# Optimization experiments

Measured on AMD Instinct MI355X. Metric: run time of the kernel, lower is better.

Reference implementation:

```python
import jax, jax.numpy as jnp
import numpy as np

DIM, HIDDEN, E = 1024, 4096, 8
B, L = 2, 2048


def setup_inputs() -> dict:
    key = jax.random.key(0)
    ks = jax.random.split(key, 6)
    s_in = 1.0 / np.sqrt(DIM)
    s_h = 1.0 / np.sqrt(HIDDEN)
    return {
        "x": jax.random.normal(ks[0], (B, L, DIM), dtype=jnp.float32),
        "Wg": jax.random.uniform(ks[1], (E, DIM), jnp.float32, -s_in, s_in),
        "W1": jax.random.uniform(ks[2], (E, DIM, HIDDEN), jnp.float32, -s_in, s_in),
        "b1": jax.random.uniform(ks[3], (E, HIDDEN), jnp.float32, -s_in, s_in),
        "W2": jax.random.uniform(ks[4], (E, HIDDEN, DIM), jnp.float32, -s_h, s_h),
        "b2": jax.random.uniform(ks[5], (E, DIM), jnp.float32, -s_h, s_h),
    }


def reference(x, Wg, W1, b1, W2, b2):
    # Router: top-1 over gate logits (softmax is monotone, argmax of probs == argmax of logits)
    gate_logits = jnp.einsum("bld,ed->ble", x, Wg)  # [B, L, E]
    top1 = jnp.argmax(gate_logits, axis=-1)          # [B, L] int
    out = jnp.zeros_like(x)
    # Fixed small loop over experts (structurally distinct weights); per-expert
    # dense MLP + select, honoring top-1 dispatch/combine semantics.
    for e in range(E):
        mask = (top1 == e)[..., None]                                   # [B, L, 1]
        h = jax.nn.gelu(jnp.einsum("bld,dh->blh", x, W1[e]) + b1[e],
                        approximate=False)                              # [B, L, H]
        y = jnp.einsum("blh,hd->bld", h, W2[e]) + b2[e]                 # [B, L, D]
        out = jnp.where(mask, y, out)
    return out
```

## Files before the change

### kernel.cpp

```cpp
#include <hip/hip_runtime.h>
#include <hip/hip_bf16.h>
#include <math.h>

#define NTOK 4096
#define DIMSZ 1024
#define HID 4096
#define NE 8
#define RT_MAX 40

typedef unsigned short u16;
typedef unsigned int u32;
typedef __attribute__((ext_vector_type(8))) short bf16x8;
typedef __attribute__((ext_vector_type(4))) float f32x4;

#define SWZ(r) (((r) >> 1) & 3)

static __device__ __forceinline__ u16 f2bf(float f) {
    u32 u = __float_as_uint(f);
    u32 r = u + 0x7fffu + ((u >> 16) & 1u);
    return (u16)(r >> 16);
}

static __device__ __forceinline__ u32 pk2bf(float lo, float hi) {
    __hip_bfloat162 h = __float22bfloat162_rn(make_float2(lo, hi));
    return *(u32*)&h;
}

__global__ void k_init(int* counts, int* cursor) {
    if (threadIdx.x < NE) { counts[threadIdx.x] = 0; cursor[threadIdx.x] = 0; }
}

__global__ void k_zero(float* p) {
    int i = blockIdx.x * 1024 + threadIdx.x * 4;
    *(float4*)(p + i) = make_float4(0.f, 0.f, 0.f, 0.f);
}

__global__ __launch_bounds__(256) void k_router(const float* __restrict__ x,
                                                const float* __restrict__ Wg,
                                                int* __restrict__ ids,
                                                int* __restrict__ counts) {
    int wave = threadIdx.x >> 6;
    int lane = threadIdx.x & 63;
    int t = blockIdx.x * 4 + wave;

    const float4* xr = (const float4*)(x + (size_t)t * DIMSZ);
    float4 xv[4];
#pragma unroll
    for (int j = 0; j < 4; j++) xv[j] = xr[j * 64 + lane];

    float s[NE];
#pragma unroll
    for (int e = 0; e < NE; e++) {
        const float4* wr = (const float4*)(Wg + (size_t)e * DIMSZ);
        float p = 0.f;
#pragma unroll
        for (int j = 0; j < 4; j++) {
            float4 w = wr[j * 64 + lane];
            p += xv[j].x * w.x + xv[j].y * w.y + xv[j].z * w.z + xv[j].w * w.w;
        }
#pragma unroll
        for (int m = 32; m >= 1; m >>= 1) p += __shfl_xor(p, m, 64);
        s[e] = p;
    }
    if (lane == 0) {
        int best = 0;
#pragma unroll
        for (int e = 1; e < NE; e++) if (s[e] > s[best]) best = e;
        ids[t] = best;
        atomicAdd(&counts[best], 1);
    }
}

__global__ void k_scan(const int* __restrict__ counts, int* __restrict__ offs) {
    if (threadIdx.x == 0) {
        int a = 0;
        for (int e = 0; e < NE; e++) { offs[e] = a; a += counts[e]; }
    }
}

__global__ __launch_bounds__(256) void k_gather(const float* __restrict__ x,
                                                const int* __restrict__ ids,
                                                const int* __restrict__ offs,
                                                int* __restrict__ cursor,
                                                int* __restrict__ perm,
                                                u16* __restrict__ Xg) {
    int t = blockIdx.x;
    __shared__ int sp;
    if (threadIdx.x == 0) {
        int e = ids[t];
        int p = offs[e] + atomicAdd(&cursor[e], 1);
        perm[p] = t;
        sp = p;
    }
    __syncthreads();
    int p = sp;
    const float4* src = (const float4*)(x + (size_t)t * DIMSZ);
    float4 v = src[threadIdx.x];
    u32 w0 = pk2bf(v.x, v.y);
    u32 w1 = pk2bf(v.z, v.w);
    uint2* dst = (uint2*)(Xg + (size_t)p * DIMSZ + threadIdx.x * 4);
    *dst = make_uint2(w0, w1);
}

__global__ __launch_bounds__(256) void k_wt(const float* __restrict__ W1,
                                            const float* __restrict__ W2,
                                            u16* __restrict__ W1T,
                                            u16* __restrict__ W2T) {
    int bid = blockIdx.x;
    const float* src;
    u16* dst;
    int K, N, kt, nt;
    if (bid < 8192) {
        int e = bid >> 10, t = bid & 1023;
        kt = t >> 6; nt = t & 63;
        src = W1 + (size_t)e * 1024 * 4096;
        dst = W1T + (size_t)e * 4096 * 1024;
        K = 1024; N = 4096;
    } else {
        int b = bid - 8192;
        int e = b >> 10, t = b & 1023;
        kt = t >> 4; nt = t & 15;
        src = W2 + (size_t)e * 4096 * 1024;
        dst = W2T + (size_t)e * 1024 * 4096;
        K = 4096; N = 1024;
    }
    __shared__ u32 T[32][65];
    int tid = threadIdx.x;
#pragma unroll
    for (int pass = 0; pass < 2; pass++) {
        int kp = (tid >> 4) + pass * 16;
        int nc = (tid & 15) * 4;
        const float* r0 = src + (size_t)(kt * 64 + 2 * kp) * N + nt * 64 + nc;
        float4 a = *(const float4*)r0;
        float4 b = *(const float4*)(r0 + N);
        T[kp][nc + 0] = pk2bf(a.x, b.x);
        T[kp][nc + 1] = pk2bf(a.y, b.y);
        T[kp][nc + 2] = pk2bf(a.z, b.z);
        T[kp][nc + 3] = pk2bf(a.w, b.w);
    }
    __syncthreads();
    int n = tid >> 2;
    int sb = (tid & 3) * 8;
    u16* orow = dst + (size_t)(nt * 64 + n) * K + kt * 64;
#pragma unroll
    for (int p = 0; p < 2; p++) {
        int s = sb + p * 4;
        uint4 w = make_uint4(T[s][n], T[s + 1][n], T[s + 2][n], T[s + 3][n]);
        *(uint4*)(orow + 2 * s) = w;
    }
}

template <int KDIM, int NDIM, int EPI, int KSPLIT>
__global__ __launch_bounds__(256, 3) void k_gemm(const u16* __restrict__ A,
                                                 const u16* __restrict__ Wt,
                                                 const float* __restrict__ biasAll,
                                                 const int* __restrict__ counts,
                                                 const int* __restrict__ offs,
                                                 const int* __restrict__ perm,
                                                 u16* __restrict__ Hout,
                                                 float* __restrict__ Fout) {
    constexpr int NT = NDIM / 128;
    constexpr int NREST = NT * KSPLIT;
    constexpr int NWG = RT_MAX * NREST;
    constexpr int CPX = NWG / 8;
    constexpr int KL = KDIM / KSPLIT;
    constexpr int NKL = KL / 32;
    int bid = blockIdx.x;
    int wid = (bid & 7) * CPX + (bid >> 3);
    int x = wid / NREST;
    int rest = wid % NREST;
    int ks = rest % KSPLIT;
    int n0 = (rest / KSPLIT) * 128;
    int kbase = ks * KL;

    int e = -1, lrt = 0, a0 = 0;
#pragma unroll
    for (int i = 0; i < NE; i++) {
        int rt = (counts[i] + 127) >> 7;
        if (e < 0 && x < a0 + rt) { e = i; lrt = x - a0; }
        a0 += rt;
    }
    if (e < 0) return;
    int row0 = offs[e] + lrt * 128;
    int nrows = offs[e] + counts[e] - row0;
    if (nrows > 128) nrows = 128;

    __shared__ alignas(16) u16 Asb[3][128][32];
    __shared__ alignas(16) u16 Bsb[3][128][32];

    int tid = threadIdx.x;
    int lane = tid & 63;
    int wave = tid >> 6;
    int wr = wave >> 1, wc = wave & 1;

    const u16* srcA[2];
    const u16* srcB[2];
#pragma unroll
    for (int p = 0; p < 2; p++) {
        int g = p * 256 + tid;
        int r = g >> 2, slot = g & 3;
        int rc = r < nrows ? r : nrows - 1;
        int kg = (slot ^ SWZ(r)) * 8;
        srcA[p] = A + (size_t)(row0 + rc) * KDIM + kbase + kg;
        srcB[p] = Wt + (size_t)e * NDIM * KDIM + (size_t)(n0 + r) * KDIM + kbase + kg;
    }

    f32x4 acc[4][4] = {};
    int fr = lane & 15, fc = lane >> 4;

    u16 *A0 = &Asb[0][0][0], *A1 = &Asb[1][0][0], *A2 = &Asb[2][0][0];
    u16 *B0 = &Bsb[0][0][0], *B1 = &Bsb[1][0][0], *B2 = &Bsb[2][0][0];

#define STAGE(AD, BD, KT)                                                       \
    {                                                                           \
        _Pragma("unroll")                                                       \
        for (int p = 0; p < 2; p++) {                                           \
            __builtin_amdgcn_global_load_lds(                                   \
                (const __attribute__((address_space(1))) void*)(srcA[p] + (size_t)(KT) * 32), \
                (__attribute__((address_space(3))) void*)((AD) + (p * 256 + wave * 64) * 8), \
                16, 0, 0);                                                      \
            __builtin_amdgcn_global_load_lds(                                   \
                (const __attribute__((address_space(1))) void*)(srcB[p] + (size_t)(KT) * 32), \
                (__attribute__((address_space(3))) void*)((BD) + (p * 256 + wave * 64) * 8), \
                16, 0, 0);                                                      \
        }                                                                       \
    }

#define COMPUTE(AP, BP)                                                         \
    {                                                                           \
        bf16x8 af[4], bfr[4];                                                   \
        _Pragma("unroll")                                                       \
        for (int m = 0; m < 4; m++) {                                           \
            int r = wr * 64 + m * 16 + fr;                                      \
            af[m] = *(const bf16x8*)((AP) + r * 32 + (fc ^ SWZ(r)) * 8);        \
        }                                                                       \
        _Pragma("unroll")                                                       \
        for (int n = 0; n < 4; n++) {                                           \
            int N = wc * 64 + n * 16 + fr;                                      \
            bfr[n] = *(const bf16x8*)((BP) + N * 32 + (fc ^ SWZ(N)) * 8);       \
        }                                                                       \
        _Pragma("unroll")                                                       \
        for (int m = 0; m < 4; m++)                                             \
            _Pragma("unroll")                                                   \
            for (int n = 0; n < 4; n++)                                         \
                acc[m][n] = __builtin_amdgcn_mfma_f32_16x16x32_bf16(af[m], bfr[n], acc[m][n], 0, 0, 0); \
    }

#define WAITV(N) asm volatile("s_waitcnt vmcnt(" #N ")" ::: "memory")
#define BAR()    __builtin_amdgcn_s_barrier()
#define SBAR()   __builtin_amdgcn_sched_barrier(0)

    STAGE(A0, B0, 0);
    STAGE(A1, B1, 1);

    for (int kk = 0; kk < NKL - 2; kk++) {
        WAITV(4);
        BAR();
        SBAR();
        STAGE(A2, B2, kk + 2);
        COMPUTE(A0, B0);
        u16* t;
        t = A0; A0 = A1; A1 = A2; A2 = t;
        t = B0; B0 = B1; B1 = B2; B2 = t;
    }
    WAITV(4);
    BAR();
    SBAR();
    COMPUTE(A0, B0);
    WAITV(0);
    BAR();
    SBAR();
    COMPUTE(A1, B1);

#undef STAGE
#undef COMPUTE
#undef WAITV
#undef BAR
#undef SBAR

    int cb = lane & 15;
    int rq = lane >> 4;
#pragma unroll
    for (int m = 0; m < 4; m++) {
        int rbase = wr * 64 + m * 16 + rq * 4;
#pragma unroll
        for (int n = 0; n < 4; n++) {
            int col = n0 + wc * 64 + n * 16 + cb;
            float bias = (EPI == 2 && ks != 0) ? 0.f : biasAll[(size_t)e * NDIM + col];
#pragma unroll
            for (int j = 0; j < 4; j++) {
                int r = rbase + j;
                if (r < nrows) {
                    float v = acc[m][n][j] + bias;
                    int p = row0 + r;
                    if (EPI == 1) {
                        float g = 0.5f * v * (1.0f + erff(v * 0.70710678118654752f));
                        Hout[(size_t)p * NDIM + col] = f2bf(g);
                    } else {
                        int trow = perm[p];
                        atomicAdd(&Fout[(size_t)trow * NDIM + col], v);
                    }
                }
            }
        }
    }
}

extern "C" void kernel_launch(void* const* d_in, const int* in_sizes, int n_in,
                              void* d_out, int out_size, void* d_ws, size_t ws_size,
                              hipStream_t stream) {
    const float* x  = (const float*)d_in[0];
    const float* Wg = (const float*)d_in[1];
    const float* W1 = (const float*)d_in[2];
    const float* b1 = (const float*)d_in[3];
    const float* W2 = (const float*)d_in[4];
    const float* b2 = (const float*)d_in[5];
    float* out = (float*)d_out;

    char* ws = (char*)d_ws;
    int* ids    = (int*)(ws + 0);
    int* counts = (int*)(ws + 16384);
    int* offs   = (int*)(ws + 16448);
    int* cursor = (int*)(ws + 16512);
    int* perm   = (int*)(ws + 16576);

    u16* Xg   = (u16*)(ws + 65536);
    u16* H    = (u16*)(ws + 65536 + 8388608);
    u16* W1T  = (u16*)(ws + 65536 + 8388608 + 33554432);
    u16* W2T  = (u16*)(ws + 65536 + 8388608 + 33554432 + 67108864);

    k_init<<<dim3(1), dim3(64), 0, stream>>>(counts, cursor);
    k_router<<<dim3(NTOK / 4), dim3(256), 0, stream>>>(x, Wg, ids, counts);
    k_scan<<<dim3(1), dim3(64), 0, stream>>>(counts, offs);
    k_gather<<<dim3(NTOK), dim3(256), 0, stream>>>(x, ids, offs, cursor, perm, Xg);
    k_wt<<<dim3(16384), dim3(256), 0, stream>>>(W1, W2, W1T, W2T);
    k_zero<<<dim3(NTOK * DIMSZ / 1024), dim3(256), 0, stream>>>(out);
    k_gemm<DIMSZ, HID, 1, 1><<<dim3(RT_MAX * (HID / 128)), dim3(256), 0, stream>>>(
        Xg, W1T, b1, counts, offs, perm, H, (float*)nullptr);
    k_gemm<HID, DIMSZ, 2, 2><<<dim3(RT_MAX * (DIMSZ / 128) * 2), dim3(256), 0, stream>>>(
        H, W2T, b2, counts, offs, perm, (u16*)nullptr, out);
}
```

Baseline: 365.7 us.

## Enlarge grouped GEMM tiles to 256x256 with 8-wave blocks and split-K pipelining

Both expert GEMMs now use 256x256 output tiles computed by 512-thread blocks. Each wave owns a 128x64 sub-tile, and a K-tile of 64 is split into two 32-wide halves that are double-buffered in LDS. Loads for the next halves are interleaved between MFMA phases, and s_setprio raises priority around the MFMA bursts. The intent is to raise arithmetic intensity and cut global and LDS traffic per FLOP. In exchange, larger tiles waste more work on partially filled expert row tiles, launch fewer workgroups, and add more barriers per K step.

Result: slower. 429.3 us (+17.4%).

```diff
diff --git a/kernel.cpp b/kernel.cpp
--- a/kernel.cpp
+++ b/kernel.cpp
@@ -6,14 +6,15 @@
 #define DIMSZ 1024
 #define HID 4096
 #define NE 8
-#define RT_MAX 40
+#define RT2 24
 
 typedef unsigned short u16;
 typedef unsigned int u32;
 typedef __attribute__((ext_vector_type(8))) short bf16x8;
 typedef __attribute__((ext_vector_type(4))) float f32x4;
 
-#define SWZ(r) (((r) >> 1) & 3)
+#define AS1 __attribute__((address_space(1)))
+#define AS3 __attribute__((address_space(3)))
 
 static __device__ __forceinline__ u16 f2bf(float f) {
     u32 u = __float_as_uint(f);
@@ -96,10 +97,8 @@
     int p = sp;
     const float4* src = (const float4*)(x + (size_t)t * DIMSZ);
     float4 v = src[threadIdx.x];
-    u32 w0 = pk2bf(v.x, v.y);
-    u32 w1 = pk2bf(v.z, v.w);
     uint2* dst = (uint2*)(Xg + (size_t)p * DIMSZ + threadIdx.x * 4);
-    *dst = make_uint2(w0, w1);
+    *dst = make_uint2(pk2bf(v.x, v.y), pk2bf(v.z, v.w));
 }
 
 __global__ __launch_bounds__(256) void k_wt(const float* __restrict__ W1,
@@ -145,13 +144,12 @@
 #pragma unroll
     for (int p = 0; p < 2; p++) {
         int s = sb + p * 4;
-        uint4 w = make_uint4(T[s][n], T[s + 1][n], T[s + 2][n], T[s + 3][n]);
-        *(uint4*)(orow + 2 * s) = w;
+        *(uint4*)(orow + 2 * s) = make_uint4(T[s][n], T[s + 1][n], T[s + 2][n], T[s + 3][n]);
     }
 }
 
 template <int KDIM, int NDIM, int EPI, int KSPLIT>
-__global__ __launch_bounds__(256, 3) void k_gemm(const u16* __restrict__ A,
+__global__ __launch_bounds__(512, 2) void k_gemm(const u16* __restrict__ A,
                                                  const u16* __restrict__ Wt,
                                                  const float* __restrict__ biasAll,
                                                  const int* __restrict__ counts,
@@ -159,130 +157,148 @@
                                                  const int* __restrict__ perm,
                                                  u16* __restrict__ Hout,
                                                  float* __restrict__ Fout) {
-    constexpr int NT = NDIM / 128;
+    constexpr int NT = NDIM / 256;
     constexpr int NREST = NT * KSPLIT;
-    constexpr int NWG = RT_MAX * NREST;
+    constexpr int NWG = RT2 * NREST;
     constexpr int CPX = NWG / 8;
     constexpr int KL = KDIM / KSPLIT;
-    constexpr int NKL = KL / 32;
+    constexpr int NKT = KL / 64;
+
     int bid = blockIdx.x;
     int wid = (bid & 7) * CPX + (bid >> 3);
     int x = wid / NREST;
     int rest = wid % NREST;
     int ks = rest % KSPLIT;
-    int n0 = (rest / KSPLIT) * 128;
+    int n0 = (rest / KSPLIT) * 256;
     int kbase = ks * KL;
 
     int e = -1, lrt = 0, a0 = 0;
 #pragma unroll
     for (int i = 0; i < NE; i++) {
-        int rt = (counts[i] + 127) >> 7;
+        int rt = (counts[i] + 255) >> 8;
         if (e < 0 && x < a0 + rt) { e = i; lrt = x - a0; }
         a0 += rt;
     }
     if (e < 0) return;
-    int row0 = offs[e] + lrt * 128;
+    int row0 = offs[e] + lrt * 256;
     int nrows = offs[e] + counts[e] - row0;
-    if (nrows > 128) nrows = 128;
-
-    __shared__ alignas(16) u16 Asb[3][128][32];
-    __shared__ alignas(16) u16 Bsb[3][128][32];
+    if (nrows > 256) nrows = 256;
+
+    __shared__ u16 Ls[2][2][2][256][32];
 
     int tid = threadIdx.x;
     int lane = tid & 63;
     int wave = tid >> 6;
-    int wr = wave >> 1, wc = wave & 1;
-
-    const u16* srcA[2];
-    const u16* srcB[2];
-#pragma unroll
-    for (int p = 0; p < 2; p++) {
-        int g = p * 256 + tid;
+    int wr = wave >> 2;
+    int wc = wave & 3;
+    int fr = lane & 15, fc = lane >> 4;
+    int gsl = fc ^ ((fr >> 1) & 3);
+
+    const u16 *sA[2], *sB[2];
+#pragma unroll
+    for (int c = 0; c < 2; c++) {
+        int g = c * 512 + tid;
         int r = g >> 2, slot = g & 3;
-        int rc = r < nrows ? r : nrows - 1;
-        int kg = (slot ^ SWZ(r)) * 8;
-        srcA[p] = A + (size_t)(row0 + rc) * KDIM + kbase + kg;
-        srcB[p] = Wt + (size_t)e * NDIM * KDIM + (size_t)(n0 + r) * KDIM + kbase + kg;
-    }
-
-    f32x4 acc[4][4] = {};
-    int fr = lane & 15, fc = lane >> 4;
-
-    u16 *A0 = &Asb[0][0][0], *A1 = &Asb[1][0][0], *A2 = &Asb[2][0][0];
-    u16 *B0 = &Bsb[0][0][0], *B1 = &Bsb[1][0][0], *B2 = &Bsb[2][0][0];
-
-#define STAGE(AD, BD, KT)                                                       \
-    {                                                                           \
-        _Pragma("unroll")                                                       \
-        for (int p = 0; p < 2; p++) {                                           \
-            __builtin_amdgcn_global_load_lds(                                   \
-                (const __attribute__((address_space(1))) void*)(srcA[p] + (size_t)(KT) * 32), \
-                (__attribute__((address_space(3))) void*)((AD) + (p * 256 + wave * 64) * 8), \
-                16, 0, 0);                                                      \
-            __builtin_amdgcn_global_load_lds(                                   \
-                (const __attribute__((address_space(1))) void*)(srcB[p] + (size_t)(KT) * 32), \
-                (__attribute__((address_space(3))) void*)((BD) + (p * 256 + wave * 64) * 8), \
-                16, 0, 0);                                                      \
-        }                                                                       \
-    }
-
-#define COMPUTE(AP, BP)                                                         \
-    {                                                                           \
-        bf16x8 af[4], bfr[4];                                                   \
-        _Pragma("unroll")                                                       \
-        for (int m = 0; m < 4; m++) {                                           \
-            int r = wr * 64 + m * 16 + fr;                                      \
-            af[m] = *(const bf16x8*)((AP) + r * 32 + (fc ^ SWZ(r)) * 8);        \
-        }                                                                       \
-        _Pragma("unroll")                                                       \
-        for (int n = 0; n < 4; n++) {                                           \
-            int N = wc * 64 + n * 16 + fr;                                      \
-            bfr[n] = *(const bf16x8*)((BP) + N * 32 + (fc ^ SWZ(N)) * 8);       \
-        }                                                                       \
-        _Pragma("unroll")                                                       \
-        for (int m = 0; m < 4; m++)                                             \
-            _Pragma("unroll")                                                   \
-            for (int n = 0; n < 4; n++)                                         \
-                acc[m][n] = __builtin_amdgcn_mfma_f32_16x16x32_bf16(af[m], bfr[n], acc[m][n], 0, 0, 0); \
-    }
-
-#define WAITV(N) asm volatile("s_waitcnt vmcnt(" #N ")" ::: "memory")
-#define BAR()    __builtin_amdgcn_s_barrier()
-#define SBAR()   __builtin_amdgcn_sched_barrier(0)
-
-    STAGE(A0, B0, 0);
-    STAGE(A1, B1, 1);
-
-    for (int kk = 0; kk < NKL - 2; kk++) {
-        WAITV(4);
-        BAR();
-        SBAR();
-        STAGE(A2, B2, kk + 2);
-        COMPUTE(A0, B0);
-        u16* t;
-        t = A0; A0 = A1; A1 = A2; A2 = t;
-        t = B0; B0 = B1; B1 = B2; B2 = t;
-    }
-    WAITV(4);
-    BAR();
-    SBAR();
-    COMPUTE(A0, B0);
-    WAITV(0);
-    BAR();
-    SBAR();
-    COMPUTE(A1, B1);
-
-#undef STAGE
-#undef COMPUTE
-#undef WAITV
+        int rc = r < nrows ? r : (nrows - 1);
+        int kg = (slot ^ ((r >> 1) & 3)) * 8;
+        sA[c] = A + (size_t)(row0 + rc) * KDIM + kbase + kg;
+        sB[c] = Wt + (size_t)e * NDIM * KDIM + (size_t)(n0 + r) * KDIM + kbase + kg;
+    }
+
+    f32x4 acc[8][4] = {};
+    bf16x8 bfr[4];
+
+#define STG(OP, SRC, BUF, S, KT)                                                  \
+    if ((KT) < NKT) {                                                             \
+        __builtin_amdgcn_global_load_lds(                                         \
+            (const AS1 void*)((SRC)[0] + (size_t)(KT) * 64 + (S) * 32),           \
+            (AS3 void*)(&Ls[BUF][OP][S][0][0] + (wave * 64) * 8), 16, 0, 0);      \
+        __builtin_amdgcn_global_load_lds(                                         \
+            (const AS1 void*)((SRC)[1] + (size_t)(KT) * 64 + (S) * 32),           \
+            (AS3 void*)(&Ls[BUF][OP][S][0][0] + (512 + wave * 64) * 8), 16, 0, 0);\
+    }
+
+#define LDA(BUF, S, H, AF)                                                        \
+    _Pragma("unroll")                                                             \
+    for (int m = 0; m < 4; m++)                                                   \
+        AF[m] = *(const bf16x8*)(&Ls[BUF][0][S][0][0] +                           \
+                 (wr * 128 + (H) * 64 + m * 16 + fr) * 32 + gsl * 8);
+
+#define LDB(BUF, S)                                                               \
+    _Pragma("unroll")                                                             \
+    for (int n = 0; n < 4; n++)                                                   \
+        bfr[n] = *(const bf16x8*)(&Ls[BUF][1][S][0][0] +                          \
+                 (wc * 64 + n * 16 + fr) * 32 + gsl * 8);
+
+#define MM(H, AF)                                                                 \
+    __builtin_amdgcn_s_setprio(1);                                                \
+    _Pragma("unroll")                                                             \
+    for (int m = 0; m < 4; m++)                                                   \
+        _Pragma("unroll")                                                         \
+        for (int n = 0; n < 4; n++)                                               \
+            acc[(H) * 4 + m][n] = __builtin_amdgcn_mfma_f32_16x16x32_bf16(        \
+                AF[m], bfr[n], acc[(H) * 4 + m][n], 0, 0, 0);                     \
+    __builtin_amdgcn_s_setprio(0);
+
+#define WL()  asm volatile("s_waitcnt lgkmcnt(0)" ::: "memory")
+#define BAR() __builtin_amdgcn_s_barrier()
+#define SCB() __builtin_amdgcn_sched_barrier(0)
+
+#define KTILE(BUF, OBUF, KT, GATE)                                                \
+    {                                                                             \
+        bf16x8 af[4];                                                             \
+                                                                          \
+        GATE; BAR(); SCB();                                                       \
+        LDA(BUF, 0, 0, af); LDB(BUF, 0);                                          \
+        STG(0, sA, OBUF, 1, (KT) + 1);                                            \
+        WL(); SCB(); MM(0, af); BAR();                                            \
+                                                                          \
+        LDA(BUF, 0, 1, af);                                                       \
+        STG(1, sB, OBUF, 1, (KT) + 1);                                            \
+        BAR(); WL(); SCB(); MM(1, af); BAR();                                     \
+                                                                          \
+        LDA(BUF, 1, 0, af); LDB(BUF, 1);                                          \
+        STG(0, sA, BUF, 0, (KT) + 2);                                             \
+        BAR(); WL(); SCB(); MM(0, af); BAR();                                     \
+                                                                          \
+        LDA(BUF, 1, 1, af);                                                       \
+        STG(1, sB, BUF, 0, (KT) + 2);                                             \
+        BAR(); WL(); SCB(); MM(1, af); BAR();                                     \
+    }
+
+#define GATE4 asm volatile("s_waitcnt vmcnt(4)" ::: "memory")
+#define GATE0 asm volatile("s_waitcnt vmcnt(0)" ::: "memory")
+
+    STG(0, sA, 0, 0, 0);
+    STG(1, sB, 0, 0, 0);
+    STG(0, sA, 0, 1, 0);
+    STG(1, sB, 0, 1, 0);
+    STG(0, sA, 1, 0, 1);
+    STG(1, sB, 1, 0, 1);
+
+    for (int t = 0; t + 3 < NKT; t += 2) {
+        KTILE(0, 1, t, GATE4);
+        KTILE(1, 0, t + 1, GATE4);
+    }
+    KTILE(0, 1, NKT - 2, GATE4);
+    KTILE(1, 0, NKT - 1, GATE0);
+
+#undef STG
+#undef LDA
+#undef LDB
+#undef MM
+#undef WL
 #undef BAR
-#undef SBAR
+#undef SCB
+#undef KTILE
+#undef GATE4
+#undef GATE0
 
     int cb = lane & 15;
     int rq = lane >> 4;
 #pragma unroll
-    for (int m = 0; m < 4; m++) {
-        int rbase = wr * 64 + m * 16 + rq * 4;
+    for (int am = 0; am < 8; am++) {
+        int rbase = wr * 128 + (am >> 2) * 64 + (am & 3) * 16 + rq * 4;
 #pragma unroll
         for (int n = 0; n < 4; n++) {
             int col = n0 + wc * 64 + n * 16 + cb;
@@ -291,14 +307,13 @@
             for (int j = 0; j < 4; j++) {
                 int r = rbase + j;
                 if (r < nrows) {
-                    float v = acc[m][n][j] + bias;
+                    float v = acc[am][n][j] + bias;
                     int p = row0 + r;
                     if (EPI == 1) {
                         float g = 0.5f * v * (1.0f + erff(v * 0.70710678118654752f));
                         Hout[(size_t)p * NDIM + col] = f2bf(g);
                     } else {
-                        int trow = perm[p];
-                        atomicAdd(&Fout[(size_t)trow * NDIM + col], v);
+                        atomicAdd(&Fout[(size_t)perm[p] * NDIM + col], v);
                     }
                 }
             }
@@ -335,8 +350,8 @@
     k_gather<<<dim3(NTOK), dim3(256), 0, stream>>>(x, ids, offs, cursor, perm, Xg);
     k_wt<<<dim3(16384), dim3(256), 0, stream>>>(W1, W2, W1T, W2T);
     k_zero<<<dim3(NTOK * DIMSZ / 1024), dim3(256), 0, stream>>>(out);
-    k_gemm<DIMSZ, HID, 1, 1><<<dim3(RT_MAX * (HID / 128)), dim3(256), 0, stream>>>(
+    k_gemm<DIMSZ, HID, 1, 1><<<dim3(RT2 * (HID / 256)), dim3(512), 0, stream>>>(
         Xg, W1T, b1, counts, offs, perm, H, (float*)nullptr);
-    k_gemm<HID, DIMSZ, 2, 2><<<dim3(RT_MAX * (DIMSZ / 128) * 2), dim3(256), 0, stream>>>(
+    k_gemm<HID, DIMSZ, 2, 2><<<dim3(RT2 * (DIMSZ / 256) * 2), dim3(512), 0, stream>>>(
         H, W2T, b2, counts, offs, perm, (u16*)nullptr, out);
 }
```

## Fuse prep kernels, overlap W2 transpose with GEMM1, double-buffer GEMMs

Applied to the files above, without the earlier changes.

Cuts the launch count by merging the gather with the W1 transpose, and merging GEMM1 with the W2 transpose and output zeroing into one grid. Per-expert offsets are now computed inline from the counts, which removes the scan kernel. The GEMM pipeline drops from triple to double buffering with an extra barrier, so LDS use falls and occupancy is raised to 5. GEMM2 split-K goes from 2 to 4. Risks are a more serialised load/compute pipeline and more output atomics.

New measurement: 453.8 us. 1.24x slower.

```diff
diff --git a/kernel.cpp b/kernel.cpp
--- a/kernel.cpp
+++ b/kernel.cpp
@@ -13,6 +13,9 @@
 typedef __attribute__((ext_vector_type(8))) short bf16x8;
 typedef __attribute__((ext_vector_type(4))) float f32x4;
 
+#define AS1 __attribute__((address_space(1)))
+#define AS3 __attribute__((address_space(3)))
+
 #define SWZ(r) (((r) >> 1) & 3)
 
 static __device__ __forceinline__ u16 f2bf(float f) {
@@ -24,15 +27,6 @@
 static __device__ __forceinline__ u32 pk2bf(float lo, float hi) {
     __hip_bfloat162 h = __float22bfloat162_rn(make_float2(lo, hi));
     return *(u32*)&h;
-}
-
-__global__ void k_init(int* counts, int* cursor) {
-    if (threadIdx.x < NE) { counts[threadIdx.x] = 0; cursor[threadIdx.x] = 0; }
-}
-
-__global__ void k_zero(float* p) {
-    int i = blockIdx.x * 1024 + threadIdx.x * 4;
-    *(float4*)(p + i) = make_float4(0.f, 0.f, 0.f, 0.f);
 }
 
 __global__ __launch_bounds__(256) void k_router(const float* __restrict__ x,
@@ -71,60 +65,10 @@
     }
 }
 
-__global__ void k_scan(const int* __restrict__ counts, int* __restrict__ offs) {
-    if (threadIdx.x == 0) {
-        int a = 0;
-        for (int e = 0; e < NE; e++) { offs[e] = a; a += counts[e]; }
-    }
-}
-
-__global__ __launch_bounds__(256) void k_gather(const float* __restrict__ x,
-                                                const int* __restrict__ ids,
-                                                const int* __restrict__ offs,
-                                                int* __restrict__ cursor,
-                                                int* __restrict__ perm,
-                                                u16* __restrict__ Xg) {
-    int t = blockIdx.x;
-    __shared__ int sp;
-    if (threadIdx.x == 0) {
-        int e = ids[t];
-        int p = offs[e] + atomicAdd(&cursor[e], 1);
-        perm[p] = t;
-        sp = p;
-    }
-    __syncthreads();
-    int p = sp;
-    const float4* src = (const float4*)(x + (size_t)t * DIMSZ);
-    float4 v = src[threadIdx.x];
-    u32 w0 = pk2bf(v.x, v.y);
-    u32 w1 = pk2bf(v.z, v.w);
-    uint2* dst = (uint2*)(Xg + (size_t)p * DIMSZ + threadIdx.x * 4);
-    *dst = make_uint2(w0, w1);
-}
-
-__global__ __launch_bounds__(256) void k_wt(const float* __restrict__ W1,
-                                            const float* __restrict__ W2,
-                                            u16* __restrict__ W1T,
-                                            u16* __restrict__ W2T) {
-    int bid = blockIdx.x;
-    const float* src;
-    u16* dst;
-    int K, N, kt, nt;
-    if (bid < 8192) {
-        int e = bid >> 10, t = bid & 1023;
-        kt = t >> 6; nt = t & 63;
-        src = W1 + (size_t)e * 1024 * 4096;
-        dst = W1T + (size_t)e * 4096 * 1024;
-        K = 1024; N = 4096;
-    } else {
-        int b = bid - 8192;
-        int e = b >> 10, t = b & 1023;
-        kt = t >> 4; nt = t & 15;
-        src = W2 + (size_t)e * 4096 * 1024;
-        dst = W2T + (size_t)e * 1024 * 4096;
-        K = 4096; N = 1024;
-    }
-    __shared__ u32 T[32][65];
+static __device__ __forceinline__ void wt_body(const float* __restrict__ src,
+                                               u16* __restrict__ dst,
+                                               int K, int N, int kt, int nt,
+                                               u32 (*T)[65]) {
     int tid = threadIdx.x;
 #pragma unroll
     for (int pass = 0; pass < 2; pass++) {
@@ -145,27 +89,26 @@
 #pragma unroll
     for (int p = 0; p < 2; p++) {
         int s = sb + p * 4;
-        uint4 w = make_uint4(T[s][n], T[s + 1][n], T[s + 2][n], T[s + 3][n]);
-        *(uint4*)(orow + 2 * s) = w;
+        *(uint4*)(orow + 2 * s) = make_uint4(T[s][n], T[s + 1][n], T[s + 2][n], T[s + 3][n]);
     }
 }
 
 template <int KDIM, int NDIM, int EPI, int KSPLIT>
-__global__ __launch_bounds__(256, 3) void k_gemm(const u16* __restrict__ A,
+static __device__ __forceinline__ void gemm_body(int bid,
+                                                 const u16* __restrict__ A,
                                                  const u16* __restrict__ Wt,
                                                  const float* __restrict__ biasAll,
                                                  const int* __restrict__ counts,
-                                                 const int* __restrict__ offs,
                                                  const int* __restrict__ perm,
                                                  u16* __restrict__ Hout,
-                                                 float* __restrict__ Fout) {
+                                                 float* __restrict__ Fout,
+                                                 u16* lds ) {
     constexpr int NT = NDIM / 128;
     constexpr int NREST = NT * KSPLIT;
     constexpr int NWG = RT_MAX * NREST;
     constexpr int CPX = NWG / 8;
     constexpr int KL = KDIM / KSPLIT;
     constexpr int NKL = KL / 32;
-    int bid = blockIdx.x;
     int wid = (bid & 7) * CPX + (bid >> 3);
     int x = wid / NREST;
     int rest = wid % NREST;
@@ -173,20 +116,22 @@
     int n0 = (rest / KSPLIT) * 128;
     int kbase = ks * KL;
 
-    int e = -1, lrt = 0, a0 = 0;
+    int e = -1, lrt = 0, a0 = 0, off_e = 0, cum = 0;
 #pragma unroll
     for (int i = 0; i < NE; i++) {
-        int rt = (counts[i] + 127) >> 7;
-        if (e < 0 && x < a0 + rt) { e = i; lrt = x - a0; }
+        int c = counts[i];
+        int rt = (c + 127) >> 7;
+        if (e < 0 && x < a0 + rt) { e = i; lrt = x - a0; off_e = cum; }
         a0 += rt;
+        cum += c;
     }
     if (e < 0) return;
-    int row0 = offs[e] + lrt * 128;
-    int nrows = offs[e] + counts[e] - row0;
+    int row0 = off_e + lrt * 128;
+    int nrows = off_e + counts[e] - row0;
     if (nrows > 128) nrows = 128;
 
-    __shared__ alignas(16) u16 Asb[3][128][32];
-    __shared__ alignas(16) u16 Bsb[3][128][32];
+    u16* Asb[2] = { lds,        lds + 8192 };
+    u16* Bsb[2] = { lds + 4096, lds + 12288 };
 
     int tid = threadIdx.x;
     int lane = tid & 63;
@@ -208,36 +153,31 @@
     f32x4 acc[4][4] = {};
     int fr = lane & 15, fc = lane >> 4;
 
-    u16 *A0 = &Asb[0][0][0], *A1 = &Asb[1][0][0], *A2 = &Asb[2][0][0];
-    u16 *B0 = &Bsb[0][0][0], *B1 = &Bsb[1][0][0], *B2 = &Bsb[2][0][0];
-
-#define STAGE(AD, BD, KT)                                                       \
+#define STAGE(BUF, KT)                                                          \
     {                                                                           \
         _Pragma("unroll")                                                       \
         for (int p = 0; p < 2; p++) {                                           \
             __builtin_amdgcn_global_load_lds(                                   \
-                (const __attribute__((address_space(1))) void*)(srcA[p] + (size_t)(KT) * 32), \
-                (__attribute__((address_space(3))) void*)((AD) + (p * 256 + wave * 64) * 8), \
-                16, 0, 0);                                                      \
+                (const AS1 void*)(srcA[p] + (size_t)(KT) * 32),                 \
+                (AS3 void*)(Asb[BUF] + (p * 256 + wave * 64) * 8), 16, 0, 0);   \
             __builtin_amdgcn_global_load_lds(                                   \
-                (const __attribute__((address_space(1))) void*)(srcB[p] + (size_t)(KT) * 32), \
-                (__attribute__((address_space(3))) void*)((BD) + (p * 256 + wave * 64) * 8), \
-                16, 0, 0);                                                      \
+                (const AS1 void*)(srcB[p] + (size_t)(KT) * 32),                 \
+                (AS3 void*)(Bsb[BUF] + (p * 256 + wave * 64) * 8), 16, 0, 0);   \
         }                                                                       \
     }
 
-#define COMPUTE(AP, BP)                                                         \
+#define COMPUTE(BUF)                                                            \
     {                                                                           \
         bf16x8 af[4], bfr[4];                                                   \
         _Pragma("unroll")                                                       \
         for (int m = 0; m < 4; m++) {                                           \
             int r = wr * 64 + m * 16 + fr;                                      \
-            af[m] = *(const bf16x8*)((AP) + r * 32 + (fc ^ SWZ(r)) * 8);        \
+            af[m] = *(const bf16x8*)(Asb[BUF] + r * 32 + (fc ^ SWZ(r)) * 8);    \
         }                                                                       \
         _Pragma("unroll")                                                       \
         for (int n = 0; n < 4; n++) {                                           \
             int N = wc * 64 + n * 16 + fr;                                      \
-            bfr[n] = *(const bf16x8*)((BP) + N * 32 + (fc ^ SWZ(N)) * 8);       \
+            bfr[n] = *(const bf16x8*)(Bsb[BUF] + N * 32 + (fc ^ SWZ(N)) * 8);   \
         }                                                                       \
         _Pragma("unroll")                                                       \
         for (int m = 0; m < 4; m++)                                             \
@@ -248,35 +188,28 @@
 
 #define WAITV(N) asm volatile("s_waitcnt vmcnt(" #N ")" ::: "memory")
 #define BAR()    __builtin_amdgcn_s_barrier()
-#define SBAR()   __builtin_amdgcn_sched_barrier(0)
-
-    STAGE(A0, B0, 0);
-    STAGE(A1, B1, 1);
-
-    for (int kk = 0; kk < NKL - 2; kk++) {
+#define SCB()    __builtin_amdgcn_sched_barrier(0)
+
+    STAGE(0, 0);
+    for (int kk = 0; kk < NKL - 1; kk++) {
+        STAGE((kk + 1) & 1, kk + 1);
         WAITV(4);
         BAR();
-        SBAR();
-        STAGE(A2, B2, kk + 2);
-        COMPUTE(A0, B0);
-        u16* t;
-        t = A0; A0 = A1; A1 = A2; A2 = t;
-        t = B0; B0 = B1; B1 = B2; B2 = t;
-    }
-    WAITV(4);
-    BAR();
-    SBAR();
-    COMPUTE(A0, B0);
+        SCB();
+        COMPUTE(kk & 1);
+        BAR();
+        SCB();
+    }
     WAITV(0);
     BAR();
-    SBAR();
-    COMPUTE(A1, B1);
+    SCB();
+    COMPUTE((NKL - 1) & 1);
 
 #undef STAGE
 #undef COMPUTE
 #undef WAITV
 #undef BAR
-#undef SBAR
+#undef SCB
 
     int cb = lane & 15;
     int rq = lane >> 4;
@@ -297,13 +230,84 @@
                         float g = 0.5f * v * (1.0f + erff(v * 0.70710678118654752f));
                         Hout[(size_t)p * NDIM + col] = f2bf(g);
                     } else {
-                        int trow = perm[p];
-                        atomicAdd(&Fout[(size_t)trow * NDIM + col], v);
+                        atomicAdd(&Fout[(size_t)perm[p] * NDIM + col], v);
                     }
                 }
             }
         }
     }
+}
+
+__global__ __launch_bounds__(256) void k_pre(const float* __restrict__ x,
+                                             const int* __restrict__ ids,
+                                             const int* __restrict__ counts,
+                                             int* __restrict__ cursor,
+                                             int* __restrict__ perm,
+                                             u16* __restrict__ Xg,
+                                             const float* __restrict__ W1,
+                                             u16* __restrict__ W1T) {
+    __shared__ u32 T[32][65];
+    __shared__ int sp;
+    int bid = blockIdx.x;
+    if (bid < NTOK) {
+        int t = bid;
+        if (threadIdx.x == 0) {
+            int e = ids[t];
+            int off = 0;
+            for (int i = 0; i < e; i++) off += counts[i];
+            int p = off + atomicAdd(&cursor[e], 1);
+            perm[p] = t;
+            sp = p;
+        }
+        __syncthreads();
+        int p = sp;
+        float4 v = ((const float4*)(x + (size_t)t * DIMSZ))[threadIdx.x];
+        *(uint2*)(Xg + (size_t)p * DIMSZ + threadIdx.x * 4) =
+            make_uint2(pk2bf(v.x, v.y), pk2bf(v.z, v.w));
+    } else {
+        int b = bid - NTOK;
+        int e = b >> 10, t = b & 1023;
+        int kt = t >> 6, nt = t & 63;
+        wt_body(W1 + (size_t)e * 1024 * 4096, W1T + (size_t)e * 4096 * 1024,
+                1024, 4096, kt, nt, T);
+    }
+}
+
+__global__ __launch_bounds__(256, 5) void k_mid(const u16* __restrict__ Xg,
+                                                const u16* __restrict__ W1T,
+                                                const float* __restrict__ b1,
+                                                const int* __restrict__ counts,
+                                                const int* __restrict__ perm,
+                                                u16* __restrict__ H,
+                                                const float* __restrict__ W2,
+                                                u16* __restrict__ W2T,
+                                                float* __restrict__ out) {
+    __shared__ alignas(16) u16 LDS[16384];
+    int bid = blockIdx.x;
+    if (bid < 1280) {
+        gemm_body<DIMSZ, HID, 1, 1>(bid, Xg, W1T, b1, counts, perm, H, (float*)nullptr, LDS);
+    } else if (bid < 1280 + 8192) {
+        int b = bid - 1280;
+        int e = b >> 10, t = b & 1023;
+        int kt = t >> 4, nt = t & 15;
+        wt_body(W2 + (size_t)e * 4096 * 1024, W2T + (size_t)e * 1024 * 4096,
+                4096, 1024, kt, nt, (u32(*)[65])LDS);
+    } else {
+        int b = bid - (1280 + 8192);
+        int i = b * 1024 + threadIdx.x * 4;
+        *(float4*)(out + i) = make_float4(0.f, 0.f, 0.f, 0.f);
+    }
+}
+
+__global__ __launch_bounds__(256, 5) void k_g2(const u16* __restrict__ H,
+                                               const u16* __restrict__ W2T,
+                                               const float* __restrict__ b2,
+                                               const int* __restrict__ counts,
+                                               const int* __restrict__ perm,
+                                               float* __restrict__ out) {
+    __shared__ alignas(16) u16 LDS[16384];
+    gemm_body<HID, DIMSZ, 2, 4>(blockIdx.x, H, W2T, b2, counts, perm,
+                                (u16*)nullptr, out, LDS);
 }
 
 extern "C" void kernel_launch(void* const* d_in, const int* in_sizes, int n_in,
@@ -320,7 +324,6 @@
     char* ws = (char*)d_ws;
     int* ids    = (int*)(ws + 0);
     int* counts = (int*)(ws + 16384);
-    int* offs   = (int*)(ws + 16448);
     int* cursor = (int*)(ws + 16512);
     int* perm   = (int*)(ws + 16576);
 
@@ -329,14 +332,9 @@
     u16* W1T  = (u16*)(ws + 65536 + 8388608 + 33554432);
     u16* W2T  = (u16*)(ws + 65536 + 8388608 + 33554432 + 67108864);
 
-    k_init<<<dim3(1), dim3(64), 0, stream>>>(counts, cursor);
+    hipMemsetAsync(ws + 16384, 0, 192, stream);
     k_router<<<dim3(NTOK / 4), dim3(256), 0, stream>>>(x, Wg, ids, counts);
-    k_scan<<<dim3(1), dim3(64), 0, stream>>>(counts, offs);
-    k_gather<<<dim3(NTOK), dim3(256), 0, stream>>>(x, ids, offs, cursor, perm, Xg);
-    k_wt<<<dim3(16384), dim3(256), 0, stream>>>(W1, W2, W1T, W2T);
-    k_zero<<<dim3(NTOK * DIMSZ / 1024), dim3(256), 0, stream>>>(out);
-    k_gemm<DIMSZ, HID, 1, 1><<<dim3(RT_MAX * (HID / 128)), dim3(256), 0, stream>>>(
-        Xg, W1T, b1, counts, offs, perm, H, (float*)nullptr);
-    k_gemm<HID, DIMSZ, 2, 2><<<dim3(RT_MAX * (DIMSZ / 128) * 2), dim3(256), 0, stream>>>(
-        H, W2T, b2, counts, offs, perm, (u16*)nullptr, out);
-}
+    k_pre<<<dim3(NTOK + 8192), dim3(256), 0, stream>>>(x, ids, counts, cursor, perm, Xg, W1, W1T);
+    k_mid<<<dim3(1280 + 8192 + 4096), dim3(256), 0, stream>>>(Xg, W1T, b1, counts, perm, H, W2, W2T, out);
+    k_g2<<<dim3(1280), dim3(256), 0, stream>>>(H, W2T, b2, counts, perm, out);
+}
```

## Enlarge expert GEMM row tile to 256 with 512-thread workgroups

Applied to the files above, without the earlier changes.

Doubles the M tile of both expert GEMMs from 128 to 256 rows, using 8 waves per workgroup so each weight tile loaded into LDS is reused across twice as many token rows. The load staging is reorganized (two A loads and one B load per thread per stage) and the vmcnt wait adjusted accordingly. This reduces weight traffic per output, but adds more padded rows for experts with partial tiles, fewer workgroups, and larger LDS use per block.

Measured after the change: 370.8 us. No clear change (+1.4%).

```diff
diff --git a/kernel.cpp b/kernel.cpp
--- a/kernel.cpp
+++ b/kernel.cpp
@@ -6,12 +6,15 @@
 #define DIMSZ 1024
 #define HID 4096
 #define NE 8
-#define RT_MAX 40
+#define RT256 24
 
 typedef unsigned short u16;
 typedef unsigned int u32;
 typedef __attribute__((ext_vector_type(8))) short bf16x8;
 typedef __attribute__((ext_vector_type(4))) float f32x4;
+
+#define AS1 __attribute__((address_space(1)))
+#define AS3 __attribute__((address_space(3)))
 
 #define SWZ(r) (((r) >> 1) & 3)
 
@@ -94,12 +97,9 @@
     }
     __syncthreads();
     int p = sp;
-    const float4* src = (const float4*)(x + (size_t)t * DIMSZ);
-    float4 v = src[threadIdx.x];
-    u32 w0 = pk2bf(v.x, v.y);
-    u32 w1 = pk2bf(v.z, v.w);
-    uint2* dst = (uint2*)(Xg + (size_t)p * DIMSZ + threadIdx.x * 4);
-    *dst = make_uint2(w0, w1);
+    float4 v = ((const float4*)(x + (size_t)t * DIMSZ))[threadIdx.x];
+    *(uint2*)(Xg + (size_t)p * DIMSZ + threadIdx.x * 4) =
+        make_uint2(pk2bf(v.x, v.y), pk2bf(v.z, v.w));
 }
 
 __global__ __launch_bounds__(256) void k_wt(const float* __restrict__ W1,
@@ -145,13 +145,12 @@
 #pragma unroll
     for (int p = 0; p < 2; p++) {
         int s = sb + p * 4;
-        uint4 w = make_uint4(T[s][n], T[s + 1][n], T[s + 2][n], T[s + 3][n]);
-        *(uint4*)(orow + 2 * s) = w;
+        *(uint4*)(orow + 2 * s) = make_uint4(T[s][n], T[s + 1][n], T[s + 2][n], T[s + 3][n]);
     }
 }
 
 template <int KDIM, int NDIM, int EPI, int KSPLIT>
-__global__ __launch_bounds__(256, 3) void k_gemm(const u16* __restrict__ A,
+__global__ __launch_bounds__(512, 4) void k_gemm(const u16* __restrict__ A,
                                                  const u16* __restrict__ Wt,
                                                  const float* __restrict__ biasAll,
                                                  const int* __restrict__ counts,
@@ -161,7 +160,7 @@
                                                  float* __restrict__ Fout) {
     constexpr int NT = NDIM / 128;
     constexpr int NREST = NT * KSPLIT;
-    constexpr int NWG = RT_MAX * NREST;
+    constexpr int NWG = RT256 * NREST;
     constexpr int CPX = NWG / 8;
     constexpr int KL = KDIM / KSPLIT;
     constexpr int NKL = KL / 32;
@@ -176,37 +175,40 @@
     int e = -1, lrt = 0, a0 = 0;
 #pragma unroll
     for (int i = 0; i < NE; i++) {
-        int rt = (counts[i] + 127) >> 7;
+        int rt = (counts[i] + 255) >> 8;
         if (e < 0 && x < a0 + rt) { e = i; lrt = x - a0; }
         a0 += rt;
     }
     if (e < 0) return;
-    int row0 = offs[e] + lrt * 128;
+    int row0 = offs[e] + lrt * 256;
     int nrows = offs[e] + counts[e] - row0;
-    if (nrows > 128) nrows = 128;
-
-    __shared__ alignas(16) u16 Asb[3][128][32];
+    if (nrows > 256) nrows = 256;
+
+    __shared__ alignas(16) u16 Asb[3][256][32];
     __shared__ alignas(16) u16 Bsb[3][128][32];
 
     int tid = threadIdx.x;
     int lane = tid & 63;
     int wave = tid >> 6;
-    int wr = wave >> 1, wc = wave & 1;
+    int wr = wave >> 1;
+    int wc = wave & 1;
+    int fr = lane & 15, fc = lane >> 4;
 
     const u16* srcA[2];
-    const u16* srcB[2];
-#pragma unroll
-    for (int p = 0; p < 2; p++) {
-        int g = p * 256 + tid;
+    const u16* srcB;
+#pragma unroll
+    for (int c = 0; c < 2; c++) {
+        int g = c * 512 + tid;
         int r = g >> 2, slot = g & 3;
         int rc = r < nrows ? r : nrows - 1;
-        int kg = (slot ^ SWZ(r)) * 8;
-        srcA[p] = A + (size_t)(row0 + rc) * KDIM + kbase + kg;
-        srcB[p] = Wt + (size_t)e * NDIM * KDIM + (size_t)(n0 + r) * KDIM + kbase + kg;
+        srcA[c] = A + (size_t)(row0 + rc) * KDIM + kbase + (slot ^ SWZ(r)) * 8;
+    }
+    {
+        int r = tid >> 2, slot = tid & 3;
+        srcB = Wt + (size_t)e * NDIM * KDIM + (size_t)(n0 + r) * KDIM + kbase + (slot ^ SWZ(r)) * 8;
     }
 
     f32x4 acc[4][4] = {};
-    int fr = lane & 15, fc = lane >> 4;
 
     u16 *A0 = &Asb[0][0][0], *A1 = &Asb[1][0][0], *A2 = &Asb[2][0][0];
     u16 *B0 = &Bsb[0][0][0], *B1 = &Bsb[1][0][0], *B2 = &Bsb[2][0][0];
@@ -214,16 +216,14 @@
 #define STAGE(AD, BD, KT)                                                       \
     {                                                                           \
         _Pragma("unroll")                                                       \
-        for (int p = 0; p < 2; p++) {                                           \
+        for (int c = 0; c < 2; c++) {                                           \
             __builtin_amdgcn_global_load_lds(                                   \
-                (const __attribute__((address_space(1))) void*)(srcA[p] + (size_t)(KT) * 32), \
-                (__attribute__((address_space(3))) void*)((AD) + (p * 256 + wave * 64) * 8), \
-                16, 0, 0);                                                      \
-            __builtin_amdgcn_global_load_lds(                                   \
-                (const __attribute__((address_space(1))) void*)(srcB[p] + (size_t)(KT) * 32), \
-                (__attribute__((address_space(3))) void*)((BD) + (p * 256 + wave * 64) * 8), \
-                16, 0, 0);                                                      \
+                (const AS1 void*)(srcA[c] + (size_t)(KT) * 32),                 \
+                (AS3 void*)((AD) + (c * 512 + wave * 64) * 8), 16, 0, 0);       \
         }                                                                       \
+        __builtin_amdgcn_global_load_lds(                                       \
+            (const AS1 void*)(srcB + (size_t)(KT) * 32),                        \
+            (AS3 void*)((BD) + (wave * 64) * 8), 16, 0, 0);                     \
     }
 
 #define COMPUTE(AP, BP)                                                         \
@@ -248,35 +248,35 @@
 
 #define WAITV(N) asm volatile("s_waitcnt vmcnt(" #N ")" ::: "memory")
 #define BAR()    __builtin_amdgcn_s_barrier()
-#define SBAR()   __builtin_amdgcn_sched_barrier(0)
+#define SCB()    __builtin_amdgcn_sched_barrier(0)
 
     STAGE(A0, B0, 0);
     STAGE(A1, B1, 1);
 
     for (int kk = 0; kk < NKL - 2; kk++) {
-        WAITV(4);
+        WAITV(3);
         BAR();
-        SBAR();
+        SCB();
         STAGE(A2, B2, kk + 2);
         COMPUTE(A0, B0);
         u16* t;
         t = A0; A0 = A1; A1 = A2; A2 = t;
         t = B0; B0 = B1; B1 = B2; B2 = t;
     }
-    WAITV(4);
+    WAITV(3);
     BAR();
-    SBAR();
+    SCB();
     COMPUTE(A0, B0);
     WAITV(0);
     BAR();
-    SBAR();
+    SCB();
     COMPUTE(A1, B1);
 
 #undef STAGE
 #undef COMPUTE
 #undef WAITV
 #undef BAR
-#undef SBAR
+#undef SCB
 
     int cb = lane & 15;
     int rq = lane >> 4;
@@ -297,8 +297,7 @@
                         float g = 0.5f * v * (1.0f + erff(v * 0.70710678118654752f));
                         Hout[(size_t)p * NDIM + col] = f2bf(g);
                     } else {
-                        int trow = perm[p];
-                        atomicAdd(&Fout[(size_t)trow * NDIM + col], v);
+                        atomicAdd(&Fout[(size_t)perm[p] * NDIM + col], v);
                     }
                 }
             }
@@ -335,8 +334,8 @@
     k_gather<<<dim3(NTOK), dim3(256), 0, stream>>>(x, ids, offs, cursor, perm, Xg);
     k_wt<<<dim3(16384), dim3(256), 0, stream>>>(W1, W2, W1T, W2T);
     k_zero<<<dim3(NTOK * DIMSZ / 1024), dim3(256), 0, stream>>>(out);
-    k_gemm<DIMSZ, HID, 1, 1><<<dim3(RT_MAX * (HID / 128)), dim3(256), 0, stream>>>(
+    k_gemm<DIMSZ, HID, 1, 1><<<dim3(RT256 * (HID / 128)), dim3(512), 0, stream>>>(
         Xg, W1T, b1, counts, offs, perm, H, (float*)nullptr);
-    k_gemm<HID, DIMSZ, 2, 2><<<dim3(RT_MAX * (DIMSZ / 128) * 2), dim3(256), 0, stream>>>(
+    k_gemm<HID, DIMSZ, 2, 2><<<dim3(RT256 * (DIMSZ / 128) * 2), dim3(512), 0, stream>>>(
         H, W2T, b2, counts, offs, perm, (u16*)nullptr, out);
 }
```
